# Performance work log

Measured on AMD Instinct MI355X. Metric: run time of the kernel, lower is better.

The kernel has to match this reference:

```python
import jax, jax.numpy as jnp
import numpy as np

V = 50257      # vocab (input_size == output_size)
H = 512        # hidden_size
T_ENC = 256    # encoder timesteps
B = 64         # batch_size (global in original code)


def lstm_cell(x, h, c, W_ih, W_hh, b_ih, b_hh):
    # torch.nn.LSTMCell: gate order i, f, g, o
    gates = x @ W_ih.T + b_ih + h @ W_hh.T + b_hh  # [B, 4H]
    i, f, g, o = jnp.split(gates, 4, axis=-1)
    i = jax.nn.sigmoid(i)
    f = jax.nn.sigmoid(f)
    g = jnp.tanh(g)
    o = jax.nn.sigmoid(o)
    c = f * c + i * g
    h = o * jnp.tanh(c)
    return h, c


def setup_inputs() -> dict:
    key = jax.random.key(0)
    ks = jax.random.split(key, 10)
    s = jnp.float32(0.02)  # small init keeps raw exp() attention in range
    emb_in = (jax.random.normal(ks[0], (V, H), jnp.float32) * s).at[0].set(0.0)   # padding_idx=0
    emb_tgt = (jax.random.normal(ks[1], (V, H), jnp.float32) * s).at[0].set(0.0)  # padding_idx=0
    W_ih = jax.random.normal(ks[2], (4 * H, H), jnp.float32) * s
    W_hh = jax.random.normal(ks[3], (4 * H, H), jnp.float32) * s
    b_ih = jax.random.normal(ks[4], (4 * H,), jnp.float32) * s
    b_hh = jax.random.normal(ks[5], (4 * H,), jnp.float32) * s
    W_out = jax.random.normal(ks[6], (V, H), jnp.float32) * s
    b_out = jax.random.normal(ks[7], (V,), jnp.float32) * s
    input_lines = jax.random.randint(ks[8], (T_ENC, B), 0, V)
    target_lines = jax.random.randint(ks[9], (2, B), 0, V)
    return dict(input_lines=input_lines, target_lines=target_lines,
                emb_in=emb_in, emb_tgt=emb_tgt,
                W_ih=W_ih, W_hh=W_hh, b_ih=b_ih, b_hh=b_hh,
                W_out=W_out, b_out=b_out)


def reference(input_lines, target_lines, emb_in, emb_tgt,
              W_ih, W_hh, b_ih, b_hh, W_out, b_out):
    B_ = input_lines.shape[1]
    H_ = emb_in.shape[1]
    xs = emb_in[input_lines]                       # [T, B, H] encoder embeddings

    def step(carry, x):
        h, c = carry
        h, c = lstm_cell(x, h, c, W_ih, W_hh, b_ih, b_hh)
        return (h, c), h

    h0 = jnp.zeros((B_, H_), xs.dtype)
    (hs, cx), hs_all = jax.lax.scan(step, (h0, h0), xs)  # hs_all: [T, B, H]

    # decoder loop body runs exactly once (break after first iteration):
    tgt0 = target_lines[0]
    logits = hs @ W_out.T + b_out                  # linear1(hs): [B, V]
    logp = jax.nn.log_softmax(logits, axis=-1)
    accum_loss = -jnp.mean(jnp.take_along_axis(logp, tgt0[:, None], axis=1)[:, 0])

    target_k = emb_tgt[tgt0]                       # [B, H]
    ht, cx = lstm_cell(target_k, hs, cx, W_ih, W_hh, b_ih, b_hh)

    # a_t: exp(ht^T @ hs_t) / sum_t exp(ht^T @ hs_t), each term [H, H]
    exp_scores = jnp.exp(jnp.einsum('bh,tbe->the', ht, hs_all))  # [T, H, H]
    at = exp_scores[0] / exp_scores.sum(axis=0)                  # [H, H]

    return accum_loss, at
```

## Files before the change

kernel.cpp:

```cpp
#include <hip/hip_runtime.h>
#include <cstdint>

#define NV 50257
#define LS 50304
#define HD 512
#define G4 2048
#define BS 64
#define TE 256

typedef float f32x4 __attribute__((ext_vector_type(4)));

__device__ __forceinline__ float sigm_f(float x) {
    x = fminf(fmaxf(x, -30.f), 30.f);
    return 1.f / (1.f + __expf(-x));
}
__device__ __forceinline__ float tanh_f(float x) {
    x = fminf(fmaxf(x, -15.f), 15.f);
    float e = __expf(2.f * x);
    return (e - 1.f) / (e + 1.f);
}

__global__ __launch_bounds__(256) void k_x(
    const int* __restrict__ lines, const int* __restrict__ tlines,
    const float* __restrict__ emb_in, const float* __restrict__ emb_tgt,
    const float* __restrict__ W_ih, const float* __restrict__ b_ih,
    const float* __restrict__ b_hh, float* __restrict__ Xbuf, int t0) {
    __shared__ float Ast[32][68];
    __shared__ float Bst[32][68];
    __shared__ const float* rowp[64];
    const int t = t0 + blockIdx.x;
    const int jt = blockIdx.y;
    const int tid = threadIdx.x;
    if (tid < 64) {
        int idx = (t < TE) ? lines[t * BS + tid] : tlines[tid];
        rowp[tid] = ((t < TE) ? emb_in : emb_tgt) + (long)idx * HD;
    }
    __syncthreads();
    const int tx = tid & 15, ty = tid >> 4;
    const int lr = tid >> 2;
    const int lc = (tid & 3) * 8;
    const float* wrow = W_ih + (long)(jt * 64 + lr) * HD + lc;
    float acc[4][4] = {};
    for (int k0 = 0; k0 < HD; k0 += 32) {
        const float* ar = rowp[lr] + k0 + lc;
        float4 a0 = *(const float4*)ar;
        float4 a1 = *(const float4*)(ar + 4);
        float4 b0 = *(const float4*)(wrow + k0);
        float4 b1 = *(const float4*)(wrow + k0 + 4);
        Ast[lc + 0][lr] = a0.x; Ast[lc + 1][lr] = a0.y;
        Ast[lc + 2][lr] = a0.z; Ast[lc + 3][lr] = a0.w;
        Ast[lc + 4][lr] = a1.x; Ast[lc + 5][lr] = a1.y;
        Ast[lc + 6][lr] = a1.z; Ast[lc + 7][lr] = a1.w;
        Bst[lc + 0][lr] = b0.x; Bst[lc + 1][lr] = b0.y;
        Bst[lc + 2][lr] = b0.z; Bst[lc + 3][lr] = b0.w;
        Bst[lc + 4][lr] = b1.x; Bst[lc + 5][lr] = b1.y;
        Bst[lc + 6][lr] = b1.z; Bst[lc + 7][lr] = b1.w;
        __syncthreads();
#pragma unroll
        for (int kk = 0; kk < 32; kk++) {
            float av[4], bv[4];
            *(float4*)av = *(const float4*)&Ast[kk][ty * 4];
            *(float4*)bv = *(const float4*)&Bst[kk][tx * 4];
#pragma unroll
            for (int i = 0; i < 4; i++)
#pragma unroll
                for (int j = 0; j < 4; j++)
                    acc[i][j] = fmaf(av[i], bv[j], acc[i][j]);
        }
        __syncthreads();
    }
    float* obase = Xbuf + ((long)blockIdx.x * BS) * G4 + jt * 64;
#pragma unroll
    for (int i = 0; i < 4; i++) {
        int r = ty * 4 + i;
        float* orow = obase + (long)r * G4;
#pragma unroll
        for (int j = 0; j < 4; j++) {
            int col = tx * 4 + j;
            int gj = jt * 64 + col;
            orow[col] = acc[i][j] + b_ih[gj] + b_hh[gj];
        }
    }
}

__device__ __forceinline__ void gbar(int* flags, int bx, int bg, int target) {
    __syncthreads();
    if (threadIdx.x == 0)
        __hip_atomic_store(&flags[bx], target, __ATOMIC_RELAXED,
                           __HIP_MEMORY_SCOPE_AGENT);
    if (threadIdx.x < 64) {
        int guard = 0;
        while (__hip_atomic_load(&flags[bg * 64 + threadIdx.x], __ATOMIC_RELAXED,
                                 __HIP_MEMORY_SCOPE_AGENT) < target) {
            __builtin_amdgcn_s_sleep(1);
            if (++guard > 2000000) break;
        }
    }
    __syncthreads();
}

__global__ __launch_bounds__(256, 1) void k_steps(
    const float* __restrict__ Xbuf, const float* __restrict__ W_hh,
    float* hs_all, float* c_buf, int* flags, int t0, int nsteps) {
    const int bx = blockIdx.x;
    const int js = bx & 63;
    const int bg = bx >> 6;
    const int tid = threadIdx.x;
    __shared__ float Wl[32][516];
    __shared__ float hl[16][516];
    __shared__ float g_lds[16][33];

    long cidx = 0;
    float creg = 0.f;
    if (tid < 128) {
        int bb = tid & 15, kk = tid >> 4;
        cidx = (long)(bg * 16 + bb) * HD + js * 8 + kk;
        creg = (t0 > 0) ? c_buf[cidx] : 0.f;
    }

    const int b = tid & 15, jj = tid >> 4;
    const int r0 = jj, r1 = jj + 16;
    const long j0 = (long)(r0 >> 3) * HD + js * 8 + (r0 & 7);
    const long j1 = (long)(r1 >> 3) * HD + js * 8 + (r1 & 7);
    const int bglob = bg * 16 + b;

#pragma unroll
    for (int m = 0; m < 16; ++m) {
        int flat = m * 256 + tid;
        int rr = flat >> 7;
        int c4 = flat & 127;
        long jrow = (long)(rr >> 3) * HD + js * 8 + (rr & 7);
        float4 v = *(const float4*)(W_hh + jrow * HD + c4 * 4);
        *(float4*)&Wl[rr][c4 * 4] = v;
    }
    __syncthreads();

    float x0 = Xbuf[(long)bglob * G4 + j0];
    float x1 = Xbuf[(long)bglob * G4 + j1];

    for (int dt = 0; dt < nsteps; ++dt) {
        const int t = t0 + dt;
        float acc0 = 0.f, acc1 = 0.f;
        if (t > 0) {
            const float* hprev = hs_all + (long)(t - 1) * BS * HD + (long)bg * 16 * HD;
            f32x4 tv[8];
#pragma unroll
            for (int m = 0; m < 8; ++m) {
                const float* a = hprev + (long)(m * 256 + tid) * 4;
                asm volatile("global_load_dwordx4 %0, %1, off sc0 sc1"
                             : "=v"(tv[m]) : "v"(a) : "memory");
            }
            asm volatile("s_waitcnt vmcnt(0)" ::: "memory");
            __builtin_amdgcn_sched_barrier(0);
#pragma unroll
            for (int m = 0; m < 8; ++m) {
                int f4 = m * 256 + tid;
                *(f32x4*)&hl[f4 >> 7][(f4 & 127) * 4] = tv[m];
            }
            __syncthreads();
#pragma unroll 8
            for (int k = 0; k < HD; k += 4) {
                float4 wa = *(const float4*)&Wl[r0][k];
                float4 wb = *(const float4*)&Wl[r1][k];
                float4 hv = *(const float4*)&hl[b][k];
                acc0 = fmaf(hv.x, wa.x, acc0); acc0 = fmaf(hv.y, wa.y, acc0);
                acc0 = fmaf(hv.z, wa.z, acc0); acc0 = fmaf(hv.w, wa.w, acc0);
                acc1 = fmaf(hv.x, wb.x, acc1); acc1 = fmaf(hv.y, wb.y, acc1);
                acc1 = fmaf(hv.z, wb.z, acc1); acc1 = fmaf(hv.w, wb.w, acc1);
            }
        }
        g_lds[b][r0] = x0 + acc0;
        g_lds[b][r1] = x1 + acc1;
        __syncthreads();
        if (tid < 128) {
            int bb = tid & 15, kk = tid >> 4;
            float gi = g_lds[bb][kk];
            float gf = g_lds[bb][8 + kk];
            float gg = g_lds[bb][16 + kk];
            float go = g_lds[bb][24 + kk];
            float iv = sigm_f(gi), fv = sigm_f(gf), gv = tanh_f(gg), ov = sigm_f(go);
            float c_new = fv * creg + iv * gv;
            creg = c_new;
            float h_new = ov * tanh_f(c_new);
            __hip_atomic_store(hs_all + (long)t * BS * HD + cidx, h_new,
                               __ATOMIC_RELAXED, __HIP_MEMORY_SCOPE_AGENT);
        }
        if (dt + 1 < nsteps) {
            const float* Xn = Xbuf + (long)(dt + 1) * BS * G4;
            x0 = Xn[(long)bglob * G4 + j0];
            x1 = Xn[(long)bglob * G4 + j1];
            gbar(flags, bx, bg, t + 1);
        } else {
            __syncthreads();
        }
    }
    if (tid < 128) c_buf[cidx] = creg;
}

__global__ __launch_bounds__(256) void k_logits(
    const float* __restrict__ hsrow, const float* __restrict__ W_out,
    const float* __restrict__ b_out, float* __restrict__ logits) {
    __shared__ float Ast[32][68];
    __shared__ float Bst[32][68];
    const int v0 = blockIdx.x * 64;
    const int tid = threadIdx.x;
    const int tx = tid & 15, ty = tid >> 4;
    const int lr = tid >> 2;
    const int lc = (tid & 3) * 8;
    int vr = v0 + lr; if (vr > NV - 1) vr = NV - 1;
    const float* arow = hsrow + (long)lr * HD + lc;
    const float* wrow = W_out + (long)vr * HD + lc;
    float acc[4][4] = {};
    for (int k0 = 0; k0 < HD; k0 += 32) {
        float4 a0 = *(const float4*)(arow + k0);
        float4 a1 = *(const float4*)(arow + k0 + 4);
        float4 b0 = *(const float4*)(wrow + k0);
        float4 b1 = *(const float4*)(wrow + k0 + 4);
        Ast[lc + 0][lr] = a0.x; Ast[lc + 1][lr] = a0.y;
        Ast[lc + 2][lr] = a0.z; Ast[lc + 3][lr] = a0.w;
        Ast[lc + 4][lr] = a1.x; Ast[lc + 5][lr] = a1.y;
        Ast[lc + 6][lr] = a1.z; Ast[lc + 7][lr] = a1.w;
        Bst[lc + 0][lr] = b0.x; Bst[lc + 1][lr] = b0.y;
        Bst[lc + 2][lr] = b0.z; Bst[lc + 3][lr] = b0.w;
        Bst[lc + 4][lr] = b1.x; Bst[lc + 5][lr] = b1.y;
        Bst[lc + 6][lr] = b1.z; Bst[lc + 7][lr] = b1.w;
        __syncthreads();
#pragma unroll
        for (int kk = 0; kk < 32; kk++) {
            float av[4], bv[4];
            *(float4*)av = *(const float4*)&Ast[kk][ty * 4];
            *(float4*)bv = *(const float4*)&Bst[kk][tx * 4];
#pragma unroll
            for (int i = 0; i < 4; i++)
#pragma unroll
                for (int j = 0; j < 4; j++)
                    acc[i][j] = fmaf(av[i], bv[j], acc[i][j]);
        }
        __syncthreads();
    }
#pragma unroll
    for (int i = 0; i < 4; i++) {
        int b = ty * 4 + i;
#pragma unroll
        for (int j = 0; j < 4; j++) {
            int v = v0 + tx * 4 + j;
            if (v < NV) logits[(long)b * LS + v] = acc[i][j] + b_out[v];
        }
    }
}

__global__ __launch_bounds__(256) void k_lse(
    const float* __restrict__ logits, float* __restrict__ lse) {
    const int b = blockIdx.x;
    const float* row = logits + (long)b * LS;
    float m = -1e30f, s = 0.f;
    for (int v = threadIdx.x; v < NV; v += 256) {
        float x = row[v];
        if (x > m) { s = s * __expf(m - x) + 1.f; m = x; }
        else s += __expf(x - m);
    }
    for (int off = 32; off; off >>= 1) {
        float m2 = __shfl_down(m, off);
        float s2 = __shfl_down(s, off);
        float M = fmaxf(m, m2);
        s = s * __expf(m - M) + s2 * __expf(m2 - M);
        m = M;
    }
    __shared__ float ms[4], ss[4];
    int wid = threadIdx.x >> 6, lane = threadIdx.x & 63;
    if (lane == 0) { ms[wid] = m; ss[wid] = s; }
    __syncthreads();
    if (threadIdx.x == 0) {
        m = ms[0]; s = ss[0];
        for (int w = 1; w < 4; w++) {
            float M = fmaxf(m, ms[w]);
            s = s * __expf(m - M) + ss[w] * __expf(ms[w] - M);
            m = M;
        }
        lse[b] = m + __logf(s);
    }
}

__global__ __launch_bounds__(64) void k_loss(
    const float* __restrict__ logits, const float* __restrict__ lse,
    const int* __restrict__ tlines, float* __restrict__ out0) {
    int b = threadIdx.x;
    float v = logits[(long)b * LS + tlines[b]] - lse[b];
    for (int off = 32; off; off >>= 1) v += __shfl_down(v, off);
    if (b == 0) out0[0] = -v * (1.f / 64.f);
}

__global__ __launch_bounds__(256) void k_attn(
    const float* __restrict__ hs, float* __restrict__ eS0, float* __restrict__ part) {
    __shared__ float Att[64][68];
    __shared__ float Bsm[64][68];
    const int hti = blockIdx.x >> 3, eti = blockIdx.x & 7;
    const int tc = blockIdx.y;
    const int tid = threadIdx.x;
    const int lb = tid >> 2;
    const int lseg = (tid & 3) * 16;
    const float* ht = hs + (long)TE * BS * HD;
    {
        const float* src = ht + (long)lb * HD + hti * 64 + lseg;
#pragma unroll
        for (int m = 0; m < 16; m += 4)
            *(float4*)&Att[lb][lseg + m] = *(const float4*)(src + m);
    }
    const int ti = tid >> 4, tj = tid & 15;
    float ps[4][4] = {};
    for (int dt = 0; dt < 64; dt++) {
        const int t = tc * 64 + dt;
        __syncthreads();
        const float* src = hs + ((long)t * BS + lb) * HD + eti * 64 + lseg;
#pragma unroll
        for (int m = 0; m < 16; m += 4)
            *(float4*)&Bsm[lb][lseg + m] = *(const float4*)(src + m);
        __syncthreads();
        float acc[4][4] = {};
#pragma unroll 4
        for (int b = 0; b < 64; b++) {
            float av[4], bv[4];
            *(float4*)av = *(const float4*)&Att[b][ti * 4];
            *(float4*)bv = *(const float4*)&Bsm[b][tj * 4];
#pragma unroll
            for (int i = 0; i < 4; i++)
#pragma unroll
                for (int j = 0; j < 4; j++)
                    acc[i][j] = fmaf(av[i], bv[j], acc[i][j]);
        }
        const bool first = (tc == 0 && dt == 0);
#pragma unroll
        for (int i = 0; i < 4; i++)
#pragma unroll
            for (int j = 0; j < 4; j++) {
                float e = __expf(acc[i][j]);
                ps[i][j] += e;
                if (first)
                    eS0[(long)(hti * 64 + ti * 4 + i) * HD + eti * 64 + tj * 4 + j] = e;
            }
    }
#pragma unroll
    for (int i = 0; i < 4; i++)
#pragma unroll
        for (int j = 0; j < 4; j++)
            part[(long)tc * 262144 + (long)(hti * 64 + ti * 4 + i) * HD + eti * 64 + tj * 4 + j] = ps[i][j];
}

__global__ __launch_bounds__(256) void k_attn_fin(
    const float* __restrict__ eS0, const float* __restrict__ part,
    float* __restrict__ outat) {
    long i = (long)blockIdx.x * 256 + threadIdx.x;
    float d = part[i] + part[262144 + i] + part[2L * 262144 + i] + part[3L * 262144 + i];
    outat[i] = eS0[i] / d;
}

extern "C" void kernel_launch(void* const* d_in, const int* in_sizes, int n_in,
                              void* d_out, int out_size, void* d_ws, size_t ws_size,
                              hipStream_t stream) {
    (void)in_sizes; (void)n_in; (void)out_size; (void)ws_size;
    const int* input_lines  = (const int*)d_in[0];
    const int* target_lines = (const int*)d_in[1];
    const float* emb_in  = (const float*)d_in[2];
    const float* emb_tgt = (const float*)d_in[3];
    const float* W_ih = (const float*)d_in[4];
    const float* W_hh = (const float*)d_in[5];
    const float* b_ih = (const float*)d_in[6];
    const float* b_hh = (const float*)d_in[7];
    const float* W_out = (const float*)d_in[8];
    const float* b_out = (const float*)d_in[9];
    float* out = (float*)d_out;
    float* ws = (float*)d_ws;

    float* X      = ws;
    float* hs     = X + 8388608;
    float* cbuf   = hs + 8421376;
    float* logits = cbuf + 32768;
    float* lse    = logits + 3219456;
    float* eS0    = lse + 64;
    float* part   = eS0 + 262144;

    int* flags = (int*)logits;
    hipMemsetAsync(flags, 0, 256 * sizeof(int), stream);

    for (int c = 0; c < 4; ++c) {
        hipLaunchKernelGGL(k_x, dim3(64, 32), dim3(256), 0, stream,
                           input_lines, target_lines, emb_in, emb_tgt,
                           W_ih, b_ih, b_hh, X, c * 64);
        hipLaunchKernelGGL(k_steps, dim3(256), dim3(256), 0, stream,
                           X, W_hh, hs, cbuf, flags, c * 64, 64);
    }
    hipLaunchKernelGGL(k_x, dim3(1, 32), dim3(256), 0, stream,
                       input_lines, target_lines, emb_in, emb_tgt,
                       W_ih, b_ih, b_hh, X, 256);
    hipLaunchKernelGGL(k_steps, dim3(256), dim3(256), 0, stream,
                       X, W_hh, hs, cbuf, flags, 256, 1);

    hipLaunchKernelGGL(k_logits, dim3(786), dim3(256), 0, stream,
                       hs + (long)255 * BS * HD, W_out, b_out, logits);
    hipLaunchKernelGGL(k_lse, dim3(64), dim3(256), 0, stream, logits, lse);
    hipLaunchKernelGGL(k_loss, dim3(1), dim3(64), 0, stream,
                       logits, lse, target_lines, out);
    hipLaunchKernelGGL(k_attn, dim3(64, 4), dim3(256), 0, stream, hs, eS0, part);
    hipLaunchKernelGGL(k_attn_fin, dim3(1024), dim3(256), 0, stream, eS0, part, out + 1);
}
```

Measured before the change: 3.220 ms.

## Keep W_hh slice in registers and split K across lanes with shuffle reduction

```diff
diff --git a/kernel.cpp b/kernel.cpp
--- a/kernel.cpp
+++ b/kernel.cpp
@@ -106,9 +106,10 @@
     const int js = bx & 63;
     const int bg = bx >> 6;
     const int tid = threadIdx.x;
-    __shared__ float Wl[32][516];
     __shared__ float hl[16][516];
     __shared__ float g_lds[16][33];
+    __shared__ float lds_pad[16384];
+    if (nsteps == -1) ((volatile float*)lds_pad)[tid] = (float)t0;
 
     long cidx = 0;
     float creg = 0.f;
@@ -118,29 +119,33 @@
         creg = (t0 > 0) ? c_buf[cidx] : 0.f;
     }
 
-    const int b = tid & 15, jj = tid >> 4;
-    const int r0 = jj, r1 = jj + 16;
-    const long j0 = (long)(r0 >> 3) * HD + js * 8 + (r0 & 7);
-    const long j1 = (long)(r1 >> 3) * HD + js * 8 + (r1 & 7);
-    const int bglob = bg * 16 + b;
-
-#pragma unroll
-    for (int m = 0; m < 16; ++m) {
-        int flat = m * 256 + tid;
-        int rr = flat >> 7;
-        int c4 = flat & 127;
-        long jrow = (long)(rr >> 3) * HD + js * 8 + (rr & 7);
-        float4 v = *(const float4*)(W_hh + jrow * HD + c4 * 4);
-        *(float4*)&Wl[rr][c4 * 4] = v;
-    }
-    __syncthreads();
-
-    float x0 = Xbuf[(long)bglob * G4 + j0];
-    float x1 = Xbuf[(long)bglob * G4 + j1];
+    const int ks = tid & 7;
+    const int bh = (tid >> 3) & 1;
+    const int r2 = tid >> 4;
+    const int ra = 2 * r2, rb = 2 * r2 + 1;
+    const long ja = (long)(ra >> 3) * HD + js * 8 + (ra & 7);
+    const long jb = (long)(rb >> 3) * HD + js * 8 + (rb & 7);
+
+    f32x4 wA[16], wB[16];
+#pragma unroll
+    for (int i = 0; i < 16; ++i) {
+        wA[i] = *(const f32x4*)(W_hh + ja * HD + 64 * ks + 4 * i);
+        wB[i] = *(const f32x4*)(W_hh + jb * HD + 64 * ks + 4 * i);
+    }
+    int sl[16];
+#pragma unroll
+    for (int i = 0; i < 16; ++i) sl[i] = 64 * ks + 4 * ((i + ks) & 15);
+
+    const int bwr = bh * 8 + ks;
+    const int bglob = bg * 16 + bwr;
+
+    float x0 = Xbuf[(long)bglob * G4 + ja];
+    float x1 = Xbuf[(long)bglob * G4 + jb];
 
     for (int dt = 0; dt < nsteps; ++dt) {
         const int t = t0 + dt;
-        float acc0 = 0.f, acc1 = 0.f;
+        float pa[8] = {0.f,0.f,0.f,0.f,0.f,0.f,0.f,0.f};
+        float pb[8] = {0.f,0.f,0.f,0.f,0.f,0.f,0.f,0.f};
         if (t > 0) {
             const float* hprev = hs_all + (long)(t - 1) * BS * HD + (long)bg * 16 * HD;
             f32x4 tv[8];
@@ -155,22 +160,47 @@
 #pragma unroll
             for (int m = 0; m < 8; ++m) {
                 int f4 = m * 256 + tid;
-                *(f32x4*)&hl[f4 >> 7][(f4 & 127) * 4] = tv[m];
+                int bb_ = f4 >> 7;
+                int c4 = f4 & 127;
+                int ksw = c4 >> 4, iw = c4 & 15;
+                *(f32x4*)&hl[bb_][64 * ksw + 4 * ((iw + ksw) & 15)] = tv[m];
             }
             __syncthreads();
-#pragma unroll 8
-            for (int k = 0; k < HD; k += 4) {
-                float4 wa = *(const float4*)&Wl[r0][k];
-                float4 wb = *(const float4*)&Wl[r1][k];
-                float4 hv = *(const float4*)&hl[b][k];
-                acc0 = fmaf(hv.x, wa.x, acc0); acc0 = fmaf(hv.y, wa.y, acc0);
-                acc0 = fmaf(hv.z, wa.z, acc0); acc0 = fmaf(hv.w, wa.w, acc0);
-                acc1 = fmaf(hv.x, wb.x, acc1); acc1 = fmaf(hv.y, wb.y, acc1);
-                acc1 = fmaf(hv.z, wb.z, acc1); acc1 = fmaf(hv.w, wb.w, acc1);
+            const float* h0 = &hl[8 * bh][0];
+#pragma unroll
+            for (int i = 0; i < 16; ++i) {
+                f32x4 hv[8];
+#pragma unroll
+                for (int bi = 0; bi < 8; ++bi)
+                    hv[bi] = *(const f32x4*)(h0 + bi * 516 + sl[i]);
+#pragma unroll
+                for (int bi = 0; bi < 8; ++bi) {
+                    pa[bi] = fmaf(hv[bi].x, wA[i].x, pa[bi]);
+                    pa[bi] = fmaf(hv[bi].y, wA[i].y, pa[bi]);
+                    pa[bi] = fmaf(hv[bi].z, wA[i].z, pa[bi]);
+                    pa[bi] = fmaf(hv[bi].w, wA[i].w, pa[bi]);
+                    pb[bi] = fmaf(hv[bi].x, wB[i].x, pb[bi]);
+                    pb[bi] = fmaf(hv[bi].y, wB[i].y, pb[bi]);
+                    pb[bi] = fmaf(hv[bi].z, wB[i].z, pb[bi]);
+                    pb[bi] = fmaf(hv[bi].w, wB[i].w, pb[bi]);
+                }
             }
-        }
-        g_lds[b][r0] = x0 + acc0;
-        g_lds[b][r1] = x1 + acc1;
+#pragma unroll
+            for (int bi = 0; bi < 8; ++bi) {
+                pa[bi] += __shfl_xor(pa[bi], 1);
+                pa[bi] += __shfl_xor(pa[bi], 2);
+                pa[bi] += __shfl_xor(pa[bi], 4);
+                pb[bi] += __shfl_xor(pb[bi], 1);
+                pb[bi] += __shfl_xor(pb[bi], 2);
+                pb[bi] += __shfl_xor(pb[bi], 4);
+            }
+        }
+        float va = pa[0], vb = pb[0];
+#pragma unroll
+        for (int j = 1; j < 8; ++j)
+            if (ks == j) { va = pa[j]; vb = pb[j]; }
+        g_lds[bwr][ra] = va + x0;
+        g_lds[bwr][rb] = vb + x1;
         __syncthreads();
         if (tid < 128) {
             int bb = tid & 15, kk = tid >> 4;
@@ -187,8 +217,8 @@
         }
         if (dt + 1 < nsteps) {
             const float* Xn = Xbuf + (long)(dt + 1) * BS * G4;
-            x0 = Xn[(long)bglob * G4 + j0];
-            x1 = Xn[(long)bglob * G4 + j1];
+            x0 = Xn[(long)bglob * G4 + ja];
+            x1 = Xn[(long)bglob * G4 + jb];
             gbar(flags, bx, bg, t + 1);
         } else {
             __syncthreads();
```

Measured after the change: 3.180 ms. About the same (-1.2%).
